# Kernel tuning notes

Hardware: AMD Instinct MI355X
Metric: run time of the kernel (lower is better)

The kernel has to match this reference:

```python
import jax, jax.numpy as jnp
import numpy as np

INPUT_DIM = 512
DEGREE = 3
NUM_KNOTS = 16
NUM_NEURONS = 1024
OUTPUT_DIM = 512
NUM_BASIS = NUM_KNOTS + DEGREE - 1  # 18


def make_knots():
    # uniform grid on [0,1], extended by `degree` knots on each side
    h = 1.0 / (NUM_KNOTS - 1)
    grid = np.linspace(0.0, 1.0, NUM_KNOTS)
    lo = grid[0] - h * np.arange(DEGREE, 0, -1)
    hi = grid[-1] + h * np.arange(1, DEGREE + 1)
    return jnp.asarray(np.concatenate([lo, grid, hi]), dtype=jnp.float32)  # [NUM_KNOTS+2*DEGREE]


def bspline_basis(x, t, degree):
    # x: [B, N]; t: [K] uniform extended knots. Cox-de Boor recursion.
    K = t.shape[0]
    xb = x[..., None]
    B = ((xb >= t[:-1]) & (xb < t[1:])).astype(x.dtype)  # [B, N, K-1]
    for p in range(1, degree + 1):
        ti = t[: K - p - 1]
        tip = t[p : K - 1]
        ti1 = t[1 : K - p]
        tip1 = t[p + 1 : K]
        left = (xb - ti) / (tip - ti) * B[..., :-1]
        right = (tip1 - xb) / (tip1 - ti1) * B[..., 1:]
        B = left + right
    return B  # [B, N, K-1-degree] == [B, N, NUM_BASIS]


def norm_layer(x, eps=1e-8):
    # per-row min-max normalization into the spline domain [0,1)
    mn = jnp.min(x, axis=-1, keepdims=True)
    mx = jnp.max(x, axis=-1, keepdims=True)
    return (x - mn) / (mx - mn + eps)


def setup_inputs() -> dict:
    key = jax.random.key(0)
    ks = jax.random.split(key, 7)
    x = jax.random.normal(ks[0], (4096, INPUT_DIM), dtype=jnp.float32)
    s1 = 1.0 / np.sqrt(INPUT_DIM)
    s2 = 1.0 / np.sqrt(NUM_NEURONS)
    W1 = jax.random.uniform(ks[1], (INPUT_DIM, NUM_NEURONS), jnp.float32, -s1, s1)
    b1 = jax.random.uniform(ks[2], (NUM_NEURONS,), jnp.float32, -s1, s1)
    coeff = jax.random.normal(ks[3], (NUM_NEURONS, NUM_BASIS), dtype=jnp.float32) * 0.1
    sp_bias = jnp.zeros((NUM_NEURONS,), dtype=jnp.float32)
    W2 = jax.random.uniform(ks[4], (NUM_NEURONS, OUTPUT_DIM), jnp.float32, -s2, s2)
    b2 = jax.random.uniform(ks[5], (OUTPUT_DIM,), jnp.float32, -s2, s2)
    return {"x": x, "W1": W1, "b1": b1, "coeff": coeff, "sp_bias": sp_bias, "W2": W2, "b2": b2}


def reference(x, W1, b1, coeff, sp_bias, W2, b2):
    t = make_knots()
    h = x @ W1 + b1                      # [B, N]  Linear 1
    h = norm_layer(h)                    # NormLayer -> [0,1)
    basis = bspline_basis(h, t, DEGREE)  # [B, N, NUM_BASIS]
    sp = jnp.einsum('bnk,nk->bn', basis, coeff) + sp_bias  # per-neuron spline eval
    out = sp @ W2 + b2                   # Linear 2
    return jax.nn.relu(out)
```

## Files before the change

### kernel.cpp

```cpp
#include <hip/hip_runtime.h>

#define M_ROWS  4096
#define IN_DIM  512
#define NEURONS 1024
#define OUT_DIM 512

typedef _Float16 f16;
typedef __attribute__((ext_vector_type(8))) _Float16 f16x8;
typedef __attribute__((ext_vector_type(4))) _Float16 f16x4;
typedef __attribute__((ext_vector_type(4))) float    f32x4;

__global__ __launch_bounds__(256) void prep(
    const float* __restrict__ x,  f16* __restrict__ xh,
    const float* __restrict__ W1, f16* __restrict__ W1t,
    const float* __restrict__ W2, f16* __restrict__ W2t,
    const float* __restrict__ coeff, const float* __restrict__ spb,
    float* __restrict__ cp)
{
    __shared__ float S[32][33];
    const int b = blockIdx.x, t = threadIdx.x;
    if (b < 1024) {
        int i = b * 256 + t;
        const float4* p = (const float4*)x;
        float4 a = p[i * 2], c = p[i * 2 + 1];
        f16x8 o = { (f16)a.x, (f16)a.y, (f16)a.z, (f16)a.w,
                    (f16)c.x, (f16)c.y, (f16)c.z, (f16)c.w };
        *(f16x8*)(xh + (size_t)i * 8) = o;
        return;
    }
    if (b < 1536) {
        const int tile = b - 1024;
        const int tx = tile & 31, ty = tile >> 5;
        const int tr = t >> 3, tc = (t & 7) * 4;
        float4 v = *(const float4*)&W1[(size_t)(ty * 32 + tr) * NEURONS + tx * 32 + tc];
        S[tr][tc + 0] = v.x; S[tr][tc + 1] = v.y;
        S[tr][tc + 2] = v.z; S[tr][tc + 3] = v.w;
        __syncthreads();
        f16x4 o = {(f16)S[tc + 0][tr], (f16)S[tc + 1][tr],
                   (f16)S[tc + 2][tr], (f16)S[tc + 3][tr]};
        *(f16x4*)&W1t[(size_t)(tx * 32 + tr) * IN_DIM + ty * 32 + tc] = o;
        return;
    }
    if (b < 2048) {
        const int tile = b - 1536;
        const int nt = tile & 15, kt2 = tile >> 4;
        const int tr = t >> 3, tc4 = (t & 7) * 4;
        float4 v = *(const float4*)&W2[(size_t)(kt2 * 32 + tr) * OUT_DIM + nt * 32 + tc4];
        S[tr][tc4 + 0] = v.x; S[tr][tc4 + 1] = v.y;
        S[tr][tc4 + 2] = v.z; S[tr][tc4 + 3] = v.w;
        __syncthreads();
        const int n = nt * 32 + tr;
        f16x4 o = {(f16)S[tc4 + 0][tr], (f16)S[tc4 + 1][tr],
                   (f16)S[tc4 + 2][tr], (f16)S[tc4 + 3][tr]};
        const int kbyte = ((kt2 * 32 + tc4) * 2) ^ ((n & 7) << 4);
        *(f16x4*)((char*)W2t + (size_t)n * 2048 + kbyte) = o;
        return;
    }
    {
        const int tid = (b - 2048) * 256 + t;
        if (tid < NEURONS * 15) {
            const int n = tid / 15, ii = tid % 15;
            const float s = spb[n];
            float4 c;
            c.x = coeff[n * 18 + ii]     + s;
            c.y = coeff[n * 18 + ii + 1] + s;
            c.z = coeff[n * 18 + ii + 2] + s;
            c.w = coeff[n * 18 + ii + 3] + s;
            *(float4*)&cp[(size_t)tid * 4] = c;
        }
    }
}

__global__ __launch_bounds__(256) void k_gemm1(
    const f16* __restrict__ A, const f16* __restrict__ Bt,
    const float* __restrict__ b1, f16* __restrict__ h,
    float* __restrict__ pmin, float* __restrict__ pmax)
{
    __shared__ f16 lds[2][(128 + 64) * 64];

    const int t    = threadIdx.x;
    const int lane = t & 63, l15 = lane & 15, lhi = lane >> 4;
    const int wid  = t >> 6;
    const int wm   = wid >> 1, wn = wid & 1;

    const int flat = blockIdx.y * gridDim.x + blockIdx.x;
    const int swz  = (flat & 7) * 64 + (flat >> 3);
    const int m0   = (swz >> 4) * 128;
    const int n0   = (swz & 15) * 64;

    auto stage = [&](int buf, int kt) {
        f16* base = &lds[buf][0];
#pragma unroll
        for (int j = 0; j < 4; ++j) {
            int c = wid * 4 + j;
            const f16* g = A + (size_t)(m0 + c * 8 + (lane >> 3)) * IN_DIM + kt + (lane & 7) * 8;
            __builtin_amdgcn_global_load_lds(
                (const __attribute__((address_space(1))) void*)g,
                (__attribute__((address_space(3))) void*)(base + c * 512), 16, 0, 0);
        }
#pragma unroll
        for (int j = 0; j < 2; ++j) {
            int c = wid * 2 + j;
            const f16* g = Bt + (size_t)(n0 + c * 8 + (lane >> 3)) * IN_DIM + kt + (lane & 7) * 8;
            __builtin_amdgcn_global_load_lds(
                (const __attribute__((address_space(1))) void*)g,
                (__attribute__((address_space(3))) void*)(base + 8192 + c * 512), 16, 0, 0);
        }
    };

    f32x4 acc[4][2];
#pragma unroll
    for (int i = 0; i < 4; ++i)
#pragma unroll
        for (int j = 0; j < 2; ++j) acc[i][j] = (f32x4)0.f;

    stage(0, 0);
    __syncthreads();

    int cur = 0;
    for (int tt = 0; tt < 8; ++tt) {
        if (tt < 7) stage(cur ^ 1, (tt + 1) * 64);
        const f16* L = &lds[cur][0];
#pragma unroll
        for (int ks = 0; ks < 2; ++ks) {
            f16x8 bfr[2];
#pragma unroll
            for (int nj = 0; nj < 2; ++nj)
                bfr[nj] = *(const f16x8*)
                    &L[8192 + (wn * 32 + nj * 16 + l15) * 64 + ks * 32 + lhi * 8];
#pragma unroll
            for (int mi = 0; mi < 4; ++mi) {
                f16x8 afr = *(const f16x8*)
                    &L[(wm * 64 + mi * 16 + l15) * 64 + ks * 32 + lhi * 8];
#pragma unroll
                for (int nj = 0; nj < 2; ++nj)
                    acc[mi][nj] = __builtin_amdgcn_mfma_f32_16x16x32_f16(
                        afr, bfr[nj], acc[mi][nj], 0, 0, 0);
            }
        }
        __syncthreads();
        cur ^= 1;
    }

    const int nb2 = (n0 >> 6) * 2 + wn;
#pragma unroll
    for (int mi = 0; mi < 4; ++mi) {
        const int row0 = m0 + wm * 64 + mi * 16 + lhi * 4;
        float vmn[4], vmx[4];
#pragma unroll
        for (int nj = 0; nj < 2; ++nj) {
            const int col = n0 + wn * 32 + nj * 16 + l15;
            const float bv = b1[col];
#pragma unroll
            for (int j = 0; j < 4; ++j) {
                f16 hv = (f16)(acc[mi][nj][j] + bv);
                h[(size_t)(row0 + j) * NEURONS + col] = hv;
                float vr = (float)hv;
                if (nj == 0) { vmn[j] = vr; vmx[j] = vr; }
                else { vmn[j] = fminf(vmn[j], vr); vmx[j] = fmaxf(vmx[j], vr); }
            }
        }
#pragma unroll
        for (int j = 0; j < 4; ++j) {
#pragma unroll
            for (int d = 1; d < 16; d <<= 1) {
                vmn[j] = fminf(vmn[j], __shfl_xor(vmn[j], d));
                vmx[j] = fmaxf(vmx[j], __shfl_xor(vmx[j], d));
            }
        }
        if (l15 == 0) {
#pragma unroll
            for (int j = 0; j < 4; ++j) {
                pmin[(size_t)nb2 * M_ROWS + row0 + j] = vmn[j];
                pmax[(size_t)nb2 * M_ROWS + row0 + j] = vmx[j];
            }
        }
    }
}

__global__ __launch_bounds__(256) void k_sp_gemm2(
    const f16* __restrict__ h, const float* __restrict__ pmin,
    const float* __restrict__ pmax, const float* __restrict__ cp,
    const f16* __restrict__ W2t, const float* __restrict__ b2,
    float* __restrict__ out)
{
    __shared__ __align__(16) f16 Bb[2][256 * 64];
    __shared__ __align__(16) f16 Aa[2][16 * 72];
    __shared__ float red[2][16][17];
    __shared__ float mnS[16], invS[16];

    const int t    = threadIdx.x;
    const int lane = t & 63, l15 = lane & 15, lhi = lane >> 4;
    const int wid  = t >> 6;

    const int flat = blockIdx.x;
    const int swz  = (flat & 7) * 64 + (flat >> 3);
    const int m0   = (swz >> 1) * 16;
    const int n0   = (swz & 1) * 256;

    {
        const int r_ = t & 15, p = t >> 4;
        const int row = m0 + r_;
        red[0][r_][p] = fminf(pmin[(size_t)p * M_ROWS + row],
                              pmin[(size_t)(p + 16) * M_ROWS + row]);
        red[1][r_][p] = fmaxf(pmax[(size_t)p * M_ROWS + row],
                              pmax[(size_t)(p + 16) * M_ROWS + row]);
    }
    __syncthreads();
    if (t < 16) {
        float a = red[0][t][0], b = red[1][t][0];
#pragma unroll
        for (int p = 1; p < 16; ++p) {
            a = fminf(a, red[0][t][p]);
            b = fmaxf(b, red[1][t][p]);
        }
        mnS[t] = a;
        invS[t] = 1.0f / (b - a + 1e-8f);
    }

    auto stageB = [&](int bf, int tt) {
        char* base = (char*)&Bb[bf][0] + wid * 8192;
#pragma unroll
        for (int j = 0; j < 8; ++j) {
            const int r = wid * 64 + j * 8 + (lane >> 3);
            const char* src = (const char*)W2t + (size_t)(n0 + r) * 2048
                              + tt * 128 + (lane & 7) * 16;
            __builtin_amdgcn_global_load_lds(
                (const __attribute__((address_space(1))) void*)src,
                (__attribute__((address_space(3))) void*)(base + j * 1024), 16, 0, 0);
        }
    };
    auto splineA = [&](int bf, int tt) {
        const int r_ = t >> 4;
        const int k4 = (t & 15) * 4;
        const int kg = tt * 64 + k4;
        f16x4 hv = *(const f16x4*)&h[(size_t)(m0 + r_) * NEURONS + kg];
        const float mn = mnS[r_], inv = invS[r_];
        f16x4 o;
#pragma unroll
        for (int e = 0; e < 4; ++e) {
            const float u   = ((float)hv[e] - mn) * inv;
            const float t15 = u * 15.0f;
            int ii = (int)t15;
            ii = ii < 0 ? 0 : (ii > 14 ? 14 : ii);
            const float tl  = t15 - (float)ii;
            const float t2  = tl * tl, t3 = t2 * tl;
            const float omt = 1.0f - tl;
            const float b0  = omt * omt * omt * (1.0f / 6.0f);
            const float b3v = t3 * (1.0f / 6.0f);
            const float b1v = (4.0f / 6.0f) - t2 + 0.5f * t3;
            const float b2v = (1.0f / 6.0f) + 0.5f * (tl + t2 - t3);
            const float4 c  = *(const float4*)&cp[((size_t)(kg + e) * 15 + ii) * 4];
            o[e] = (f16)(c.x * b0 + c.y * b1v + c.z * b2v + c.w * b3v);
        }
        *(f16x4*)&Aa[bf][r_ * 72 + k4] = o;
    };

    f32x4 acc[4];
#pragma unroll
    for (int j = 0; j < 4; ++j) acc[j] = (f32x4)0.f;

    stageB(0, 0);
    __syncthreads();
    splineA(0, 0);
    __syncthreads();

    int cur = 0;
    for (int tt = 0; tt < 16; ++tt) {
        if (tt < 15) {
            stageB(cur ^ 1, tt + 1);
            splineA(cur ^ 1, tt + 1);
        }
        const char* B_ = (const char*)&Bb[cur][0];
#pragma unroll
        for (int ks = 0; ks < 2; ++ks) {
            f16x8 afr = *(const f16x8*)&Aa[cur][l15 * 72 + ks * 32 + lhi * 8];
#pragma unroll
            for (int nj = 0; nj < 4; ++nj) {
                const int cl = wid * 64 + nj * 16 + l15;
                const int kb = (ks * 64 + lhi * 16) ^ ((cl & 7) << 4);
                f16x8 bfr = *(const f16x8*)(B_ + (size_t)cl * 128 + kb);
                acc[nj] = __builtin_amdgcn_mfma_f32_16x16x32_f16(afr, bfr, acc[nj], 0, 0, 0);
            }
        }
        __syncthreads();
        cur ^= 1;
    }

#pragma unroll
    for (int nj = 0; nj < 4; ++nj) {
        const int col = n0 + wid * 64 + nj * 16 + l15;
        const float bv = b2[col];
        const int row0 = m0 + lhi * 4;
#pragma unroll
        for (int j = 0; j < 4; ++j)
            out[(size_t)(row0 + j) * OUT_DIM + col] = fmaxf(acc[nj][j] + bv, 0.0f);
    }
}

extern "C" void kernel_launch(void* const* d_in, const int* in_sizes, int n_in,
                              void* d_out, int out_size, void* d_ws, size_t ws_size,
                              hipStream_t stream)
{
    const float* x     = (const float*)d_in[0];
    const float* W1    = (const float*)d_in[1];
    const float* b1    = (const float*)d_in[2];
    const float* coeff = (const float*)d_in[3];
    const float* spb   = (const float*)d_in[4];
    const float* W2    = (const float*)d_in[5];
    const float* b2    = (const float*)d_in[6];
    float* out = (float*)d_out;

    char* ws = (char*)d_ws;
    f16*   h    = (f16*)ws;
    f16*   xh   = (f16*)(ws + ( 8u << 20));
    f16*   W1t  = (f16*)(ws + (12u << 20));
    f16*   W2t  = (f16*)(ws + (13u << 20));
    float* pmin = (float*)(ws + (14u << 20));
    float* pmax = (float*)(ws + (14u << 20) + (512u << 10));
    float* cp   = (float*)(ws + (15u << 20));

    prep<<<dim3(2108), 256, 0, stream>>>(x, xh, W1, W1t, W2, W2t, coeff, spb, cp);

    k_gemm1<<<dim3(16, 32), 256, 0, stream>>>(xh, W1t, b1, h, pmin, pmax);

    k_sp_gemm2<<<dim3(512), 256, 0, stream>>>(h, pmin, pmax, cp, W2t, b2, out);
}
```

Baseline: 50.04 us.

## Split fused spline+GEMM2 into separate spline kernel and square-tiled GEMM2

```diff
diff --git a/kernel.cpp b/kernel.cpp
--- a/kernel.cpp
+++ b/kernel.cpp
@@ -44,16 +44,14 @@
     if (b < 2048) {
         const int tile = b - 1536;
         const int nt = tile & 15, kt2 = tile >> 4;
-        const int tr = t >> 3, tc4 = (t & 7) * 4;
-        float4 v = *(const float4*)&W2[(size_t)(kt2 * 32 + tr) * OUT_DIM + nt * 32 + tc4];
-        S[tr][tc4 + 0] = v.x; S[tr][tc4 + 1] = v.y;
-        S[tr][tc4 + 2] = v.z; S[tr][tc4 + 3] = v.w;
+        const int tr = t >> 3, tc = (t & 7) * 4;
+        float4 v = *(const float4*)&W2[(size_t)(kt2 * 32 + tr) * OUT_DIM + nt * 32 + tc];
+        S[tr][tc + 0] = v.x; S[tr][tc + 1] = v.y;
+        S[tr][tc + 2] = v.z; S[tr][tc + 3] = v.w;
         __syncthreads();
-        const int n = nt * 32 + tr;
-        f16x4 o = {(f16)S[tc4 + 0][tr], (f16)S[tc4 + 1][tr],
-                   (f16)S[tc4 + 2][tr], (f16)S[tc4 + 3][tr]};
-        const int kbyte = ((kt2 * 32 + tc4) * 2) ^ ((n & 7) << 4);
-        *(f16x4*)((char*)W2t + (size_t)n * 2048 + kbyte) = o;
+        f16x4 o = {(f16)S[tc + 0][tr], (f16)S[tc + 1][tr],
+                   (f16)S[tc + 2][tr], (f16)S[tc + 3][tr]};
+        *(f16x4*)&W2t[(size_t)(nt * 32 + tr) * NEURONS + kt2 * 32 + tc] = o;
         return;
     }
     {
@@ -178,67 +176,31 @@
     }
 }
 
-__global__ __launch_bounds__(256) void k_sp_gemm2(
+__global__ __launch_bounds__(256) void k_spline(
     const f16* __restrict__ h, const float* __restrict__ pmin,
     const float* __restrict__ pmax, const float* __restrict__ cp,
-    const f16* __restrict__ W2t, const float* __restrict__ b2,
-    float* __restrict__ out)
-{
-    __shared__ __align__(16) f16 Bb[2][256 * 64];
-    __shared__ __align__(16) f16 Aa[2][16 * 72];
-    __shared__ float red[2][16][17];
-    __shared__ float mnS[16], invS[16];
-
+    f16* __restrict__ sph)
+{
     const int t    = threadIdx.x;
-    const int lane = t & 63, l15 = lane & 15, lhi = lane >> 4;
-    const int wid  = t >> 6;
-
-    const int flat = blockIdx.x;
-    const int swz  = (flat & 7) * 64 + (flat >> 3);
-    const int m0   = (swz >> 1) * 16;
-    const int n0   = (swz & 1) * 256;
-
-    {
-        const int r_ = t & 15, p = t >> 4;
-        const int row = m0 + r_;
-        red[0][r_][p] = fminf(pmin[(size_t)p * M_ROWS + row],
-                              pmin[(size_t)(p + 16) * M_ROWS + row]);
-        red[1][r_][p] = fmaxf(pmax[(size_t)p * M_ROWS + row],
-                              pmax[(size_t)(p + 16) * M_ROWS + row]);
-    }
-    __syncthreads();
-    if (t < 16) {
-        float a = red[0][t][0], b = red[1][t][0];
-#pragma unroll
-        for (int p = 1; p < 16; ++p) {
-            a = fminf(a, red[0][t][p]);
-            b = fmaxf(b, red[1][t][p]);
-        }
-        mnS[t] = a;
-        invS[t] = 1.0f / (b - a + 1e-8f);
-    }
-
-    auto stageB = [&](int bf, int tt) {
-        char* base = (char*)&Bb[bf][0] + wid * 8192;
-#pragma unroll
-        for (int j = 0; j < 8; ++j) {
-            const int r = wid * 64 + j * 8 + (lane >> 3);
-            const char* src = (const char*)W2t + (size_t)(n0 + r) * 2048
-                              + tt * 128 + (lane & 7) * 16;
-            __builtin_amdgcn_global_load_lds(
-                (const __attribute__((address_space(1))) void*)src,
-                (__attribute__((address_space(3))) void*)(base + j * 1024), 16, 0, 0);
-        }
-    };
-    auto splineA = [&](int bf, int tt) {
-        const int r_ = t >> 4;
-        const int k4 = (t & 15) * 4;
-        const int kg = tt * 64 + k4;
-        f16x4 hv = *(const f16x4*)&h[(size_t)(m0 + r_) * NEURONS + kg];
-        const float mn = mnS[r_], inv = invS[r_];
-        f16x4 o;
-#pragma unroll
-        for (int e = 0; e < 4; ++e) {
+    const int lane = t & 63;
+    const int row  = blockIdx.x * 4 + (t >> 6);
+
+    float mn = pmin[(size_t)(lane & 31) * M_ROWS + row];
+    float mx = pmax[(size_t)(lane & 31) * M_ROWS + row];
+#pragma unroll
+    for (int d = 1; d < 32; d <<= 1) {
+        mn = fminf(mn, __shfl_xor(mn, d));
+        mx = fmaxf(mx, __shfl_xor(mx, d));
+    }
+    const float inv = 1.0f / (mx - mn + 1e-8f);
+
+#pragma unroll
+    for (int half = 0; half < 2; ++half) {
+        const int k0 = half * 512 + lane * 8;
+        f16x8 hv = *(const f16x8*)&h[(size_t)row * NEURONS + k0];
+        f16x8 o;
+#pragma unroll
+        for (int e = 0; e < 8; ++e) {
             const float u   = ((float)hv[e] - mn) * inv;
             const float t15 = u * 15.0f;
             int ii = (int)t15;
@@ -250,37 +212,77 @@
             const float b3v = t3 * (1.0f / 6.0f);
             const float b1v = (4.0f / 6.0f) - t2 + 0.5f * t3;
             const float b2v = (1.0f / 6.0f) + 0.5f * (tl + t2 - t3);
-            const float4 c  = *(const float4*)&cp[((size_t)(kg + e) * 15 + ii) * 4];
+            const float4 c  = *(const float4*)&cp[((size_t)(k0 + e) * 15 + ii) * 4];
             o[e] = (f16)(c.x * b0 + c.y * b1v + c.z * b2v + c.w * b3v);
         }
-        *(f16x4*)&Aa[bf][r_ * 72 + k4] = o;
+        *(f16x8*)&sph[(size_t)row * NEURONS + k0] = o;
+    }
+}
+
+__global__ __launch_bounds__(256) void k_gemm2(
+    const f16* __restrict__ A, const f16* __restrict__ Bt,
+    const float* __restrict__ b2, float* __restrict__ out)
+{
+    __shared__ f16 lds[2][128 * 128];
+
+    const int t    = threadIdx.x;
+    const int lane = t & 63, l15 = lane & 15, lhi = lane >> 4;
+    const int wid  = t >> 6;
+    const int wm   = wid >> 1, wn = wid & 1;
+
+    const int flat = blockIdx.x;
+    const int swz  = (flat & 7) * 64 + (flat >> 3);
+    const int m0   = (swz >> 3) * 64;
+    const int n0   = (swz & 7) * 64;
+
+    auto stage = [&](int buf, int kt) {
+        f16* base = &lds[buf][0];
+#pragma unroll
+        for (int j = 0; j < 4; ++j) {
+            int c = wid * 4 + j;
+            const f16* g = A + (size_t)(m0 + c * 4 + (lane >> 4)) * NEURONS + kt + (lane & 15) * 8;
+            __builtin_amdgcn_global_load_lds(
+                (const __attribute__((address_space(1))) void*)g,
+                (__attribute__((address_space(3))) void*)(base + c * 512), 16, 0, 0);
+        }
+#pragma unroll
+        for (int j = 0; j < 4; ++j) {
+            int c = wid * 4 + j;
+            const f16* g = Bt + (size_t)(n0 + c * 4 + (lane >> 4)) * NEURONS + kt + (lane & 15) * 8;
+            __builtin_amdgcn_global_load_lds(
+                (const __attribute__((address_space(1))) void*)g,
+                (__attribute__((address_space(3))) void*)(base + 8192 + c * 512), 16, 0, 0);
+        }
     };
 
-    f32x4 acc[4];
-#pragma unroll
-    for (int j = 0; j < 4; ++j) acc[j] = (f32x4)0.f;
-
-    stageB(0, 0);
+    f32x4 acc[2][2];
+#pragma unroll
+    for (int i = 0; i < 2; ++i)
+#pragma unroll
+        for (int j = 0; j < 2; ++j) acc[i][j] = (f32x4)0.f;
+
+    stage(0, 0);
     __syncthreads();
-    splineA(0, 0);
-    __syncthreads();
 
     int cur = 0;
-    for (int tt = 0; tt < 16; ++tt) {
-        if (tt < 15) {
-            stageB(cur ^ 1, tt + 1);
-            splineA(cur ^ 1, tt + 1);
-        }
-        const char* B_ = (const char*)&Bb[cur][0];
-#pragma unroll
-        for (int ks = 0; ks < 2; ++ks) {
-            f16x8 afr = *(const f16x8*)&Aa[cur][l15 * 72 + ks * 32 + lhi * 8];
-#pragma unroll
-            for (int nj = 0; nj < 4; ++nj) {
-                const int cl = wid * 64 + nj * 16 + l15;
-                const int kb = (ks * 64 + lhi * 16) ^ ((cl & 7) << 4);
-                f16x8 bfr = *(const f16x8*)(B_ + (size_t)cl * 128 + kb);
-                acc[nj] = __builtin_amdgcn_mfma_f32_16x16x32_f16(afr, bfr, acc[nj], 0, 0, 0);
+    for (int tt = 0; tt < 8; ++tt) {
+        if (tt < 7) stage(cur ^ 1, (tt + 1) * 128);
+        const f16* L = &lds[cur][0];
+#pragma unroll
+        for (int ks = 0; ks < 4; ++ks) {
+            f16x8 bfr[2];
+#pragma unroll
+            for (int nj = 0; nj < 2; ++nj)
+                bfr[nj] = *(const f16x8*)
+                    &L[8192 + (wn * 32 + nj * 16 + l15) * 128 + ks * 32 + lhi * 8];
+#pragma unroll
+            for (int mi = 0; mi < 2; ++mi) {
+                f16x8 afr = *(const f16x8*)
+                    &L[(wm * 32 + mi * 16 + l15) * 128 + ks * 32 + lhi * 8];
+#pragma unroll
+                for (int nj = 0; nj < 2; ++nj)
+                    acc[mi][nj] = __builtin_amdgcn_mfma_f32_16x16x32_f16(
+                        afr, bfr[nj], acc[mi][nj], 0, 0, 0);
             }
         }
         __syncthreads();
@@ -288,13 +290,17 @@
     }
 
 #pragma unroll
-    for (int nj = 0; nj < 4; ++nj) {
-        const int col = n0 + wid * 64 + nj * 16 + l15;
-        const float bv = b2[col];
-        const int row0 = m0 + lhi * 4;
-#pragma unroll
-        for (int j = 0; j < 4; ++j)
-            out[(size_t)(row0 + j) * OUT_DIM + col] = fmaxf(acc[nj][j] + bv, 0.0f);
+    for (int mi = 0; mi < 2; ++mi) {
+        const int row0 = m0 + wm * 32 + mi * 16 + lhi * 4;
+#pragma unroll
+        for (int nj = 0; nj < 2; ++nj) {
+            const int col = n0 + wn * 32 + nj * 16 + l15;
+            const float bv = b2[col];
+#pragma unroll
+            for (int j = 0; j < 4; ++j)
+                out[(size_t)(row0 + j) * OUT_DIM + col] =
+                    fmaxf(acc[mi][nj][j] + bv, 0.0f);
+        }
     }
 }
 
@@ -313,16 +319,19 @@
 
     char* ws = (char*)d_ws;
     f16*   h    = (f16*)ws;
-    f16*   xh   = (f16*)(ws + ( 8u << 20));
-    f16*   W1t  = (f16*)(ws + (12u << 20));
-    f16*   W2t  = (f16*)(ws + (13u << 20));
-    float* pmin = (float*)(ws + (14u << 20));
-    float* pmax = (float*)(ws + (14u << 20) + (512u << 10));
-    float* cp   = (float*)(ws + (15u << 20));
+    f16*   sph  = (f16*)(ws + ( 8u << 20));
+    f16*   xh   = (f16*)(ws + (16u << 20));
+    f16*   W1t  = (f16*)(ws + (20u << 20));
+    f16*   W2t  = (f16*)(ws + (21u << 20));
+    float* pmin = (float*)(ws + (22u << 20));
+    float* pmax = (float*)(ws + (22u << 20) + (512u << 10));
+    float* cp   = (float*)(ws + (23u << 20));
 
     prep<<<dim3(2108), 256, 0, stream>>>(x, xh, W1, W1t, W2, W2t, coeff, spb, cp);
 
     k_gemm1<<<dim3(16, 32), 256, 0, stream>>>(xh, W1t, b1, h, pmin, pmax);
 
-    k_sp_gemm2<<<dim3(512), 256, 0, stream>>>(h, pmin, pmax, cp, W2t, b2, out);
-}
+    k_spline<<<dim3(1024), 256, 0, stream>>>(h, pmin, pmax, cp, sph);
+
+    k_gemm2<<<dim3(512), 256, 0, stream>>>(sph, W2t, b2, out);
+}
```

Result: slower. 53.80 us (+7.5%).
